# Kernel optimization log

Hardware: AMD Instinct MI355X
Metric: run time of the kernel (lower is better)

The kernel has to match this reference:

```python
import jax, jax.numpy as jnp
import numpy as np
from jax import lax


def setup_inputs() -> dict:
    key = jax.random.key(0)
    ks = jax.random.split(key, 5)
    D, S, T, B, H = 2, 48, 48, 32, 256
    std = 1.0 / np.sqrt(H)
    return {
        "src_input_seq": jax.random.normal(ks[0], (S, B, H), jnp.float32),
        "trg_input_seq": jax.random.normal(ks[1], (T, B, H), jnp.float32),
        "W": jax.random.uniform(ks[2], (D, H, H), jnp.float32, -std, std),
        "U": jax.random.uniform(ks[3], (D, 2 * H, H), jnp.float32, -std, std),
        "b": jax.random.uniform(ks[4], (D, 1, H), jnp.float32, -std, std),
    }


def _grid_layer(x, y, Wd, Ud, bd):
    # x, y: [S, T, B, H] per-cell inputs for this depth
    S, T, B, H = x.shape
    Ux, Uy = Ud[:H], Ud[H:]  # state = concat([state_x, state_y]) @ U

    def row_step(prev_row_hx, row_inputs):
        # prev_row_hx: [T, B, H] = h_x of row i-1 (state_x); zeros for i == 0
        x_row, y_row = row_inputs  # [T, B, H]

        def cell_step(left_hx, inp):
            # left_hx: [B, H] = h_x of cell (i, j-1) (state_y); zeros for j == 0
            up_hx, x_t, y_t = inp
            temp = up_hx @ Ux + left_hx @ Uy + bd  # [B, H]
            h_x = jnp.tanh(x_t @ Wd + temp)
            h_y = jnp.tanh(y_t @ Wd + temp)
            return h_x, (h_x, h_y)

        _, (hx_row, hy_row) = lax.scan(
            cell_step, jnp.zeros((B, H), x.dtype), (prev_row_hx, x_row, y_row)
        )
        return hx_row, (hx_row, hy_row)

    _, (HX, HY) = lax.scan(row_step, jnp.zeros((T, B, H), x.dtype), (x, y))
    return jnp.stack([HX, HY], axis=2)  # [S, T, 2, B, H]


def reference(src_input_seq, trg_input_seq, W, U, b):
    S, B, H = src_input_seq.shape
    T = trg_input_seq.shape[0]
    depth = W.shape[0]
    # depth-0 inputs: x_t = src[i] (same for all j), y_t = trg[j] (same for all i)
    xs = jnp.broadcast_to(src_input_seq[:, None], (S, T, B, H))
    ys = jnp.broadcast_to(trg_input_seq[None, :], (S, T, B, H))
    outs = []
    for d in range(depth):
        Hd = _grid_layer(xs, ys, W[d], U[d], b[d])  # [S, T, 2, B, H]
        outs.append(Hd)
        xs, ys = Hd[:, :, 0], Hd[:, :, 1]
    return jnp.stack(outs, axis=0)  # [depth, S, T, 2, B, H]
```

## Files before the change

### kernel.cpp

```cpp
#include <hip/hip_runtime.h>
#include <hip/hip_bf16.h>


typedef short short8 __attribute__((ext_vector_type(8)));
typedef float f32x4 __attribute__((ext_vector_type(4)));

static constexpr size_t UF_OFF    = 0;
static constexpr size_t WF_OFF    = 512u * 1024;
static constexpr size_t SRCW_OFF  = 768u * 1024;
static constexpr size_t TRGW_OFF  = SRCW_OFF + 48u * 32 * 256 * 4;
static constexpr size_t FLAG0_OFF = TRGW_OFF + 48u * 32 * 256 * 4;
static constexpr size_t FLAG1_OFF = FLAG0_OFF + 48u * 48 * 4;

#define MFMA16(a, b, c) __builtin_amdgcn_mfma_f32_16x16x32_bf16(a, b, c, 0, 0, 0)

__device__ __forceinline__ short f2bf(float f) {
  __hip_bfloat16 h = __float2bfloat16(f);
  return __builtin_bit_cast(short, h);
}

__device__ __forceinline__ size_t plane_off(int d, int s, int t, int c) {
  return (size_t)(((d * 48 + s) * 48 + t) * 2 + c) * 8192u;
}

__device__ __forceinline__ void wait_ge(int* p, int v) {
  while (__hip_atomic_load(p, __ATOMIC_RELAXED, __HIP_MEMORY_SCOPE_AGENT) < v)
    __builtin_amdgcn_s_sleep(1);
  asm volatile("" ::: "memory");
}

__device__ __forceinline__ void st_llc(float* p, float v) {
  __hip_atomic_store(p, v, __ATOMIC_RELAXED, __HIP_MEMORY_SCOPE_AGENT);
}

__device__ __forceinline__ float fast_tanh(float x) {
  float e = exp2f(x * 2.88539008f);
  return 1.f - __fdividef(2.f, e + 1.f);
}

__global__ void preswizzle(const float* __restrict__ U,
                           const float* __restrict__ W,
                           char* __restrict__ ws) {
  int gid = blockIdx.x * 256 + threadIdx.x;
  if (gid < 32768) {
    int r = gid >> 11;
    int d = r >> 3, nh = (r >> 2) & 1, w = r & 3;
    int c = gid & 2047;
    int f = c >> 6, lane = c & 63;
    int nt = f >> 4, ks = f & 15;
    int kbase = ks * 32 + (lane >> 4) * 8;
    int n = nh * 128 + w * 32 + nt * 16 + (lane & 15);
    const float* sp = U + (size_t)d * 512 * 256 + n;
    short8 v;
#pragma unroll
    for (int j = 0; j < 8; ++j) v[j] = f2bf(sp[(size_t)(kbase + j) * 256]);
    *(short8*)(ws + UF_OFF + (size_t)gid * 16) = v;
  } else {
    int idx = gid - 32768;
    int r = idx >> 10;
    int d = r >> 3, nh = (r >> 2) & 1, w = r & 3;
    int c = idx & 1023;
    int f = c >> 6, lane = c & 63;
    int nt = f >> 3, ks = f & 7;
    int kbase = ks * 32 + (lane >> 4) * 8;
    int n = nh * 128 + w * 32 + nt * 16 + (lane & 15);
    const float* sp = W + (size_t)d * 256 * 256 + n;
    short8 v;
#pragma unroll
    for (int j = 0; j < 8; ++j) v[j] = f2bf(sp[(size_t)(kbase + j) * 256]);
    *(short8*)(ws + WF_OFF + (size_t)idx * 16) = v;
  }
}

__global__ __launch_bounds__(256, 1) void precompute_xw(
    const float* __restrict__ src, const float* __restrict__ trg,
    const float* __restrict__ bvec, char* __restrict__ ws) {
  __shared__ __align__(16) char lds[32 * 528];
  const int bid = blockIdx.x;
  const int i = bid >> 1, nh = bid & 1;
  const int tid = threadIdx.x;
  const int w = tid >> 6, lane = tid & 63;
  const int alane = lane & 15, q = lane >> 4;

  short8 bw[2][8];
  {
    const char* wb = ws + WF_OFF + (size_t)(nh * 4 + w) * 16384u + (size_t)lane * 16;
#pragma unroll
    for (int nt = 0; nt < 2; ++nt)
#pragma unroll
      for (int ks = 0; ks < 8; ++ks)
        bw[nt][ks] = *(const short8*)(wb + (nt * 8 + ks) * 1024);
  }

  const float* plane = (i < 48) ? src + (size_t)i * 8192 : trg + (size_t)(i - 48) * 8192;
#pragma unroll
  for (int it = 0; it < 4; ++it) {
    int gid = it * 256 + tid;
    int row = gid >> 5, c = gid & 31;
    const float* p = plane + row * 256 + c * 8;
    short8 v;
#pragma unroll
    for (int j = 0; j < 8; ++j) v[j] = f2bf(p[j]);
    *(short8*)(lds + row * 528 + c * 16) = v;
  }
  __syncthreads();

  const f32x4 zf = {0.f, 0.f, 0.f, 0.f};
  f32x4 acc[2][2];
  acc[0][0] = zf; acc[0][1] = zf; acc[1][0] = zf; acc[1][1] = zf;
  const char* ar0 = lds + alane * 528 + q * 16;
  const char* ar1 = lds + (alane + 16) * 528 + q * 16;
#pragma unroll
  for (int ks = 0; ks < 8; ++ks) {
    short8 a0 = *(const short8*)(ar0 + ks * 64);
    short8 a1 = *(const short8*)(ar1 + ks * 64);
#pragma unroll
    for (int nt = 0; nt < 2; ++nt) {
      acc[0][nt] = MFMA16(a0, bw[nt][ks], acc[0][nt]);
      acc[1][nt] = MFMA16(a1, bw[nt][ks], acc[1][nt]);
    }
  }

  const int n0 = nh * 128 + w * 32 + alane;
  float bs[2] = {bvec[n0], bvec[n0 + 16]};
  float* dst = (float*)(ws + (i < 48 ? SRCW_OFF : TRGW_OFF)) +
               (size_t)(i < 48 ? i : i - 48) * 8192;
#pragma unroll
  for (int mt = 0; mt < 2; ++mt)
#pragma unroll
    for (int nt = 0; nt < 2; ++nt)
#pragma unroll
      for (int rr = 0; rr < 4; ++rr) {
        int row = mt * 16 + q * 4 + rr;
        dst[row * 256 + n0 + nt * 16] = acc[mt][nt][rr] + bs[nt];
      }
}

__global__ __launch_bounds__(256, 1) void grid_main(
    float* __restrict__ out, const float* __restrict__ bvec,
    char* __restrict__ ws) {
  __shared__ __align__(16) char lds[32 * 1040];
  const int bid = blockIdx.x;
  const int d = bid / 96;
  const int r = bid % 96;
  const int t = r >> 1, nh = r & 1;
  const int tid = threadIdx.x;
  const int w = tid >> 6, lane = tid & 63;
  const int alane = lane & 15, q = lane >> 4;

  int* flag0 = (int*)(ws + FLAG0_OFF);
  int* flag1 = (int*)(ws + FLAG1_OFF);
  const float* SRCW = (const float*)(ws + SRCW_OFF);
  const float* TRGW = (const float*)(ws + TRGW_OFF);

  short8 bu[2][16];
  {
    const char* ub = ws + UF_OFF + (size_t)((d * 2 + nh) * 4 + w) * 32768u + (size_t)lane * 16;
#pragma unroll
    for (int nt = 0; nt < 2; ++nt)
#pragma unroll
      for (int ks = 0; ks < 16; ++ks)
        bu[nt][ks] = *(const short8*)(ub + (nt * 16 + ks) * 1024);
  }
  short8 bw[2][8];
  float bs1[2] = {0.f, 0.f};
  if (d == 1) {
    const char* wb = ws + WF_OFF + (size_t)((2 + nh) * 4 + w) * 16384u + (size_t)lane * 16;
#pragma unroll
    for (int nt = 0; nt < 2; ++nt)
#pragma unroll
      for (int ks = 0; ks < 8; ++ks)
        bw[nt][ks] = *(const short8*)(wb + (nt * 8 + ks) * 1024);
    int bn = nh * 128 + w * 32 + alane;
    bs1[0] = bvec[256 + bn];
    bs1[1] = bvec[256 + bn + 16];
  }

  const char* ar0 = lds + alane * 1040 + q * 16;
  const char* ar1 = lds + (alane + 16) * 1040 + q * 16;
  const int n0 = nh * 128 + w * 32 + alane;
  const f32x4 zf = {0.f, 0.f, 0.f, 0.f};

  for (int s = 0; s < 48; ++s) {
    f32x4 acc[2][2];
    acc[0][0] = zf; acc[0][1] = zf; acc[1][0] = zf; acc[1][1] = zf;

    if (d == 0) {
      float pfx[16], pfy[16];
      {
        const float* sxp = SRCW + (size_t)s * 8192;
        const float* syp = TRGW + (size_t)t * 8192;
#pragma unroll
        for (int mt = 0; mt < 2; ++mt)
#pragma unroll
          for (int nt = 0; nt < 2; ++nt)
#pragma unroll
            for (int rr = 0; rr < 4; ++rr) {
              int row = mt * 16 + q * 4 + rr;
              int n = n0 + nt * 16;
              pfx[(mt * 2 + nt) * 4 + rr] = sxp[row * 256 + n];
              pfy[(mt * 2 + nt) * 4 + rr] = syp[row * 256 + n];
            }
      }
      if (s > 0) wait_ge(&flag0[(s - 1) * 48 + t], 2);
      if (t > 0) wait_ge(&flag0[s * 48 + (t - 1)], 2);
      {
        const float* pu = (s > 0) ? out + plane_off(0, s - 1, t, 0) : nullptr;
        const float* pl = (t > 0) ? out + plane_off(0, s, t - 1, 0) : nullptr;
#pragma unroll
        for (int it = 0; it < 8; ++it) {
          int gid = it * 256 + tid;
          int p = gid >> 10, row = (gid >> 5) & 31, c = gid & 31;
          const float* pp = p ? pl : pu;
          short8 v = {0, 0, 0, 0, 0, 0, 0, 0};
          if (pp) {
#pragma unroll
            for (int j = 0; j < 8; ++j) v[j] = f2bf(pp[row * 256 + c * 8 + j]);
          }
          *(short8*)(lds + row * 1040 + (p * 32 + c) * 16) = v;
        }
      }
      __syncthreads();
#pragma unroll
      for (int ks = 0; ks < 16; ++ks) {
        short8 a0 = *(const short8*)(ar0 + ks * 64);
        short8 a1 = *(const short8*)(ar1 + ks * 64);
#pragma unroll
        for (int nt = 0; nt < 2; ++nt) {
          acc[0][nt] = MFMA16(a0, bu[nt][ks], acc[0][nt]);
          acc[1][nt] = MFMA16(a1, bu[nt][ks], acc[1][nt]);
        }
      }
      float* hxp = out + plane_off(0, s, t, 0);
      float* hyp = out + plane_off(0, s, t, 1);
#pragma unroll
      for (int mt = 0; mt < 2; ++mt)
#pragma unroll
        for (int nt = 0; nt < 2; ++nt)
#pragma unroll
          for (int rr = 0; rr < 4; ++rr) {
            int row = mt * 16 + q * 4 + rr;
            int n = n0 + nt * 16;
            int i = (mt * 2 + nt) * 4 + rr;
            float tv = acc[mt][nt][rr];
            st_llc(&hxp[row * 256 + n], fast_tanh(pfx[i] + tv));
            st_llc(&hyp[row * 256 + n], fast_tanh(pfy[i] + tv));
          }
    } else {
      wait_ge(&flag0[s * 48 + t], 2);
      {
        const float* px = out + plane_off(0, s, t, 0);
        const float* py = out + plane_off(0, s, t, 1);
#pragma unroll
        for (int it = 0; it < 8; ++it) {
          int gid = it * 256 + tid;
          int p = gid >> 10, row = (gid >> 5) & 31, c = gid & 31;
          const float* pp = p ? py : px;
          short8 v;
#pragma unroll
          for (int j = 0; j < 8; ++j) v[j] = f2bf(pp[row * 256 + c * 8 + j]);
          *(short8*)(lds + row * 1040 + (p * 32 + c) * 16) = v;
        }
      }
      __syncthreads();
      f32x4 accx[2][2], accy[2][2];
      accx[0][0] = zf; accx[0][1] = zf; accx[1][0] = zf; accx[1][1] = zf;
      accy[0][0] = zf; accy[0][1] = zf; accy[1][0] = zf; accy[1][1] = zf;
#pragma unroll
      for (int ks = 0; ks < 8; ++ks) {
        short8 ax0 = *(const short8*)(ar0 + ks * 64);
        short8 ax1 = *(const short8*)(ar1 + ks * 64);
        short8 ay0 = *(const short8*)(ar0 + 512 + ks * 64);
        short8 ay1 = *(const short8*)(ar1 + 512 + ks * 64);
#pragma unroll
        for (int nt = 0; nt < 2; ++nt) {
          accx[0][nt] = MFMA16(ax0, bw[nt][ks], accx[0][nt]);
          accx[1][nt] = MFMA16(ax1, bw[nt][ks], accx[1][nt]);
          accy[0][nt] = MFMA16(ay0, bw[nt][ks], accy[0][nt]);
          accy[1][nt] = MFMA16(ay1, bw[nt][ks], accy[1][nt]);
        }
      }
      __syncthreads();
      if (s > 0) wait_ge(&flag1[(s - 1) * 48 + t], 2);
      if (t > 0) wait_ge(&flag1[s * 48 + (t - 1)], 2);
      {
        const float* pu = (s > 0) ? out + plane_off(1, s - 1, t, 0) : nullptr;
        const float* pl = (t > 0) ? out + plane_off(1, s, t - 1, 0) : nullptr;
#pragma unroll
        for (int it = 0; it < 8; ++it) {
          int gid = it * 256 + tid;
          int p = gid >> 10, row = (gid >> 5) & 31, c = gid & 31;
          const float* pp = p ? pl : pu;
          short8 v = {0, 0, 0, 0, 0, 0, 0, 0};
          if (pp) {
#pragma unroll
            for (int j = 0; j < 8; ++j) v[j] = f2bf(pp[row * 256 + c * 8 + j]);
          }
          *(short8*)(lds + row * 1040 + (p * 32 + c) * 16) = v;
        }
      }
      __syncthreads();
#pragma unroll
      for (int ks = 0; ks < 16; ++ks) {
        short8 a0 = *(const short8*)(ar0 + ks * 64);
        short8 a1 = *(const short8*)(ar1 + ks * 64);
#pragma unroll
        for (int nt = 0; nt < 2; ++nt) {
          acc[0][nt] = MFMA16(a0, bu[nt][ks], acc[0][nt]);
          acc[1][nt] = MFMA16(a1, bu[nt][ks], acc[1][nt]);
        }
      }
      float* hxp = out + plane_off(1, s, t, 0);
      float* hyp = out + plane_off(1, s, t, 1);
#pragma unroll
      for (int mt = 0; mt < 2; ++mt)
#pragma unroll
        for (int nt = 0; nt < 2; ++nt)
#pragma unroll
          for (int rr = 0; rr < 4; ++rr) {
            int row = mt * 16 + q * 4 + rr;
            int n = n0 + nt * 16;
            float tv = acc[mt][nt][rr];
            st_llc(&hxp[row * 256 + n], fast_tanh(accx[mt][nt][rr] + tv + bs1[nt]));
            hyp[row * 256 + n] = fast_tanh(accy[mt][nt][rr] + tv + bs1[nt]);
          }
    }
    asm volatile("s_waitcnt vmcnt(0)" ::: "memory");
    __syncthreads();
    if (tid == 0) {
      int* fp = (d == 0) ? &flag0[s * 48 + t] : &flag1[s * 48 + t];
      __hip_atomic_fetch_add(fp, 1, __ATOMIC_RELAXED, __HIP_MEMORY_SCOPE_AGENT);
    }
  }
}

extern "C" void kernel_launch(void* const* d_in, const int* in_sizes, int n_in,
                              void* d_out, int out_size, void* d_ws, size_t ws_size,
                              hipStream_t stream) {
  const float* src = (const float*)d_in[0];
  const float* trg = (const float*)d_in[1];
  const float* W   = (const float*)d_in[2];
  const float* U   = (const float*)d_in[3];
  const float* bv  = (const float*)d_in[4];
  float* out = (float*)d_out;
  char* ws = (char*)d_ws;

  hipMemsetAsync(ws + FLAG0_OFF, 0, 2u * 48 * 48 * 4, stream);
  preswizzle<<<192, 256, 0, stream>>>(U, W, ws);
  precompute_xw<<<192, 256, 0, stream>>>(src, trg, bv, ws);
  grid_main<<<192, 256, 0, stream>>>(out, bv, ws);
}
```

Measured before the change: 964.5 us.

## Merge column halves into one block and keep the up-state in LDS

Each block now owns a whole t-column (both N halves, 512 threads) instead of half of one. The block keeps its own previous-row h_x in LDS as bf16, so only the left neighbour has to be fetched from global memory after a flag wait. Flags are padded to separate cache lines and counted per wave (8 arrivals). Depth-1 W fragments are read from global inside the loop rather than held in registers. This shortens the cross-block dependency chain and halves the global traffic per cell. The cost is fewer blocks (96) and heavier per-block work, including duplicated MFMAs for the x and y accumulators at depth 0.

```diff
diff --git a/kernel.cpp b/kernel.cpp
--- a/kernel.cpp
+++ b/kernel.cpp
@@ -10,7 +10,8 @@
 static constexpr size_t SRCW_OFF  = 768u * 1024;
 static constexpr size_t TRGW_OFF  = SRCW_OFF + 48u * 32 * 256 * 4;
 static constexpr size_t FLAG0_OFF = TRGW_OFF + 48u * 32 * 256 * 4;
-static constexpr size_t FLAG1_OFF = FLAG0_OFF + 48u * 48 * 4;
+static constexpr size_t FLAG1_OFF = FLAG0_OFF + 48u * 48 * 128;
+static constexpr int    FSTRIDE   = 32;
 
 #define MFMA16(a, b, c) __builtin_amdgcn_mfma_f32_16x16x32_bf16(a, b, c, 0, 0, 0)
 
@@ -136,60 +137,127 @@
       }
 }
 
-__global__ __launch_bounds__(256, 1) void grid_main(
+__global__ __launch_bounds__(512, 2) void grid_main(
     float* __restrict__ out, const float* __restrict__ bvec,
     char* __restrict__ ws) {
-  __shared__ __align__(16) char lds[32 * 1040];
+  __shared__ __align__(16) char lds[3 * 32 * 528];
+  char* const buf0 = lds;
+  char* const buf1 = lds + 32 * 528;
+  char* const buf2 = lds + 2 * 32 * 528;
+
   const int bid = blockIdx.x;
-  const int d = bid / 96;
-  const int r = bid % 96;
-  const int t = r >> 1, nh = r & 1;
+  const int d = bid / 48;
+  const int t = bid % 48;
   const int tid = threadIdx.x;
-  const int w = tid >> 6, lane = tid & 63;
+  const int wv = tid >> 6;
+  const int nh = wv >> 2, w = wv & 3;
+  const int lane = tid & 63;
   const int alane = lane & 15, q = lane >> 4;
+  const int n0 = nh * 128 + w * 32 + alane;
 
   int* flag0 = (int*)(ws + FLAG0_OFF);
   int* flag1 = (int*)(ws + FLAG1_OFF);
   const float* SRCW = (const float*)(ws + SRCW_OFF);
   const float* TRGW = (const float*)(ws + TRGW_OFF);
 
+  for (int i = tid; i < 32 * 528 / 4; i += 512) ((int*)buf0)[i] = 0;
+
   short8 bu[2][16];
   {
-    const char* ub = ws + UF_OFF + (size_t)((d * 2 + nh) * 4 + w) * 32768u + (size_t)lane * 16;
+    const char* ub = ws + UF_OFF + (size_t)((d * 2 + nh) * 4 + w) * 32768u +
+                     (size_t)lane * 16;
 #pragma unroll
     for (int nt = 0; nt < 2; ++nt)
 #pragma unroll
       for (int ks = 0; ks < 16; ++ks)
         bu[nt][ks] = *(const short8*)(ub + (nt * 16 + ks) * 1024);
   }
-  short8 bw[2][8];
-  float bs1[2] = {0.f, 0.f};
-  if (d == 1) {
-    const char* wb = ws + WF_OFF + (size_t)((2 + nh) * 4 + w) * 16384u + (size_t)lane * 16;
-#pragma unroll
-    for (int nt = 0; nt < 2; ++nt)
-#pragma unroll
-      for (int ks = 0; ks < 8; ++ks)
-        bw[nt][ks] = *(const short8*)(wb + (nt * 8 + ks) * 1024);
-    int bn = nh * 128 + w * 32 + alane;
-    bs1[0] = bvec[256 + bn];
-    bs1[1] = bvec[256 + bn + 16];
-  }
-
-  const char* ar0 = lds + alane * 1040 + q * 16;
-  const char* ar1 = lds + (alane + 16) * 1040 + q * 16;
-  const int n0 = nh * 128 + w * 32 + alane;
-  const f32x4 zf = {0.f, 0.f, 0.f, 0.f};
-
-  for (int s = 0; s < 48; ++s) {
-    f32x4 acc[2][2];
-    acc[0][0] = zf; acc[0][1] = zf; acc[1][0] = zf; acc[1][1] = zf;
-
-    if (d == 0) {
-      float pfx[16], pfy[16];
+
+  const char* up0 = buf0 + alane * 528 + q * 16;
+  const char* up1 = buf0 + (alane + 16) * 528 + q * 16;
+  const char* l0  = buf1 + alane * 528 + q * 16;
+  const char* l1  = buf1 + (alane + 16) * 528 + q * 16;
+  const char* y0  = buf2 + alane * 528 + q * 16;
+  const char* y1  = buf2 + (alane + 16) * 528 + q * 16;
+
+  __syncthreads();
+
+  if (d == 0) {
+    float pfy[16];
+    {
+      const float* syp = TRGW + (size_t)t * 8192;
+#pragma unroll
+      for (int mt = 0; mt < 2; ++mt)
+#pragma unroll
+        for (int nt = 0; nt < 2; ++nt)
+#pragma unroll
+          for (int rr = 0; rr < 4; ++rr) {
+            int row = mt * 16 + q * 4 + rr;
+            pfy[(mt * 2 + nt) * 4 + rr] = syp[row * 256 + n0 + nt * 16];
+          }
+    }
+    for (int s = 0; s < 48; ++s) {
+      f32x4 accx[2][2], accy[2][2];
       {
         const float* sxp = SRCW + (size_t)s * 8192;
-        const float* syp = TRGW + (size_t)t * 8192;
+#pragma unroll
+        for (int mt = 0; mt < 2; ++mt)
+#pragma unroll
+          for (int nt = 0; nt < 2; ++nt)
+#pragma unroll
+            for (int rr = 0; rr < 4; ++rr) {
+              int row = mt * 16 + q * 4 + rr;
+              accx[mt][nt][rr] = sxp[row * 256 + n0 + nt * 16];
+              accy[mt][nt][rr] = pfy[(mt * 2 + nt) * 4 + rr];
+            }
+      }
+      if (t > 0) {
+        wait_ge(&flag0[(s * 48 + (t - 1)) * FSTRIDE], 8);
+        const float* pl = out + plane_off(0, s, t - 1, 0);
+#pragma unroll
+        for (int it = 0; it < 2; ++it) {
+          int gid = it * 512 + tid;
+          int row = gid >> 5, c = gid & 31;
+          const float* p = pl + row * 256 + c * 8;
+          short8 v;
+#pragma unroll
+          for (int j = 0; j < 8; ++j) v[j] = f2bf(p[j]);
+          *(short8*)(buf1 + row * 528 + c * 16) = v;
+        }
+      }
+      __syncthreads();
+#pragma unroll
+      for (int ks = 0; ks < 8; ++ks) {
+        short8 a0 = *(const short8*)(up0 + ks * 64);
+        short8 a1 = *(const short8*)(up1 + ks * 64);
+        accx[0][0] = MFMA16(a0, bu[0][ks], accx[0][0]);
+        accx[0][1] = MFMA16(a0, bu[1][ks], accx[0][1]);
+        accx[1][0] = MFMA16(a1, bu[0][ks], accx[1][0]);
+        accx[1][1] = MFMA16(a1, bu[1][ks], accx[1][1]);
+        accy[0][0] = MFMA16(a0, bu[0][ks], accy[0][0]);
+        accy[0][1] = MFMA16(a0, bu[1][ks], accy[0][1]);
+        accy[1][0] = MFMA16(a1, bu[0][ks], accy[1][0]);
+        accy[1][1] = MFMA16(a1, bu[1][ks], accy[1][1]);
+      }
+      if (t > 0) {
+#pragma unroll
+        for (int ks = 0; ks < 8; ++ks) {
+          short8 a0 = *(const short8*)(l0 + ks * 64);
+          short8 a1 = *(const short8*)(l1 + ks * 64);
+          accx[0][0] = MFMA16(a0, bu[0][8 + ks], accx[0][0]);
+          accx[0][1] = MFMA16(a0, bu[1][8 + ks], accx[0][1]);
+          accx[1][0] = MFMA16(a1, bu[0][8 + ks], accx[1][0]);
+          accx[1][1] = MFMA16(a1, bu[1][8 + ks], accx[1][1]);
+          accy[0][0] = MFMA16(a0, bu[0][8 + ks], accy[0][0]);
+          accy[0][1] = MFMA16(a0, bu[1][8 + ks], accy[0][1]);
+          accy[1][0] = MFMA16(a1, bu[0][8 + ks], accy[1][0]);
+          accy[1][1] = MFMA16(a1, bu[1][8 + ks], accy[1][1]);
+        }
+      }
+      float hx[16];
+      {
+        float* hxp = out + plane_off(0, s, t, 0);
+        float* hyp = out + plane_off(0, s, t, 1);
 #pragma unroll
         for (int mt = 0; mt < 2; ++mt)
 #pragma unroll
@@ -198,41 +266,18 @@
             for (int rr = 0; rr < 4; ++rr) {
               int row = mt * 16 + q * 4 + rr;
               int n = n0 + nt * 16;
-              pfx[(mt * 2 + nt) * 4 + rr] = sxp[row * 256 + n];
-              pfy[(mt * 2 + nt) * 4 + rr] = syp[row * 256 + n];
+              float xv = fast_tanh(accx[mt][nt][rr]);
+              float yv = fast_tanh(accy[mt][nt][rr]);
+              hx[(mt * 2 + nt) * 4 + rr] = xv;
+              st_llc(&hxp[row * 256 + n], xv);
+              st_llc(&hyp[row * 256 + n], yv);
             }
       }
-      if (s > 0) wait_ge(&flag0[(s - 1) * 48 + t], 2);
-      if (t > 0) wait_ge(&flag0[s * 48 + (t - 1)], 2);
-      {
-        const float* pu = (s > 0) ? out + plane_off(0, s - 1, t, 0) : nullptr;
-        const float* pl = (t > 0) ? out + plane_off(0, s, t - 1, 0) : nullptr;
-#pragma unroll
-        for (int it = 0; it < 8; ++it) {
-          int gid = it * 256 + tid;
-          int p = gid >> 10, row = (gid >> 5) & 31, c = gid & 31;
-          const float* pp = p ? pl : pu;
-          short8 v = {0, 0, 0, 0, 0, 0, 0, 0};
-          if (pp) {
-#pragma unroll
-            for (int j = 0; j < 8; ++j) v[j] = f2bf(pp[row * 256 + c * 8 + j]);
-          }
-          *(short8*)(lds + row * 1040 + (p * 32 + c) * 16) = v;
-        }
-      }
-      __syncthreads();
-#pragma unroll
-      for (int ks = 0; ks < 16; ++ks) {
-        short8 a0 = *(const short8*)(ar0 + ks * 64);
-        short8 a1 = *(const short8*)(ar1 + ks * 64);
-#pragma unroll
-        for (int nt = 0; nt < 2; ++nt) {
-          acc[0][nt] = MFMA16(a0, bu[nt][ks], acc[0][nt]);
-          acc[1][nt] = MFMA16(a1, bu[nt][ks], acc[1][nt]);
-        }
-      }
-      float* hxp = out + plane_off(0, s, t, 0);
-      float* hyp = out + plane_off(0, s, t, 1);
+      asm volatile("s_waitcnt vmcnt(0)" ::: "memory");
+      if (lane == 0)
+        __hip_atomic_fetch_add(&flag0[(s * 48 + t) * FSTRIDE], 1,
+                               __ATOMIC_RELAXED, __HIP_MEMORY_SCOPE_AGENT);
+      __syncthreads();
 #pragma unroll
       for (int mt = 0; mt < 2; ++mt)
 #pragma unroll
@@ -240,78 +285,120 @@
 #pragma unroll
           for (int rr = 0; rr < 4; ++rr) {
             int row = mt * 16 + q * 4 + rr;
-            int n = n0 + nt * 16;
-            int i = (mt * 2 + nt) * 4 + rr;
-            float tv = acc[mt][nt][rr];
-            st_llc(&hxp[row * 256 + n], fast_tanh(pfx[i] + tv));
-            st_llc(&hyp[row * 256 + n], fast_tanh(pfy[i] + tv));
+            *(short*)(buf0 + row * 528 + (n0 + nt * 16) * 2) =
+                f2bf(hx[(mt * 2 + nt) * 4 + rr]);
           }
-    } else {
-      wait_ge(&flag0[s * 48 + t], 2);
+      __syncthreads();
+    }
+  } else {
+    const char* wb = ws + WF_OFF + (size_t)((2 + nh) * 4 + w) * 16384u +
+                     (size_t)lane * 16;
+    const float bsa = bvec[256 + n0], bsb = bvec[256 + n0 + 16];
+    const f32x4 bA = {bsa, bsa, bsa, bsa};
+    const f32x4 bB = {bsb, bsb, bsb, bsb};
+    const f32x4 zf = {0.f, 0.f, 0.f, 0.f};
+    for (int s = 0; s < 48; ++s) {
+      f32x4 accx[2][2], accy[2][2], acc[2][2];
+      accx[0][0] = bA; accx[0][1] = bB; accx[1][0] = bA; accx[1][1] = bB;
+      accy[0][0] = bA; accy[0][1] = bB; accy[1][0] = bA; accy[1][1] = bB;
+      acc[0][0] = zf; acc[0][1] = zf; acc[1][0] = zf; acc[1][1] = zf;
+
+      wait_ge(&flag0[(s * 48 + t) * FSTRIDE], 8);
       {
         const float* px = out + plane_off(0, s, t, 0);
         const float* py = out + plane_off(0, s, t, 1);
 #pragma unroll
-        for (int it = 0; it < 8; ++it) {
-          int gid = it * 256 + tid;
-          int p = gid >> 10, row = (gid >> 5) & 31, c = gid & 31;
-          const float* pp = p ? py : px;
+        for (int it = 0; it < 4; ++it) {
+          int gid = it * 512 + tid;
+          int pidx = gid >> 10, row = (gid >> 5) & 31, c = gid & 31;
+          const float* pp = pidx ? py : px;
+          char* db = pidx ? buf2 : buf1;
+          const float* p = pp + row * 256 + c * 8;
           short8 v;
 #pragma unroll
-          for (int j = 0; j < 8; ++j) v[j] = f2bf(pp[row * 256 + c * 8 + j]);
-          *(short8*)(lds + row * 1040 + (p * 32 + c) * 16) = v;
+          for (int j = 0; j < 8; ++j) v[j] = f2bf(p[j]);
+          *(short8*)(db + row * 528 + c * 16) = v;
         }
       }
       __syncthreads();
-      f32x4 accx[2][2], accy[2][2];
-      accx[0][0] = zf; accx[0][1] = zf; accx[1][0] = zf; accx[1][1] = zf;
-      accy[0][0] = zf; accy[0][1] = zf; accy[1][0] = zf; accy[1][1] = zf;
 #pragma unroll
       for (int ks = 0; ks < 8; ++ks) {
-        short8 ax0 = *(const short8*)(ar0 + ks * 64);
-        short8 ax1 = *(const short8*)(ar1 + ks * 64);
-        short8 ay0 = *(const short8*)(ar0 + 512 + ks * 64);
-        short8 ay1 = *(const short8*)(ar1 + 512 + ks * 64);
-#pragma unroll
-        for (int nt = 0; nt < 2; ++nt) {
-          accx[0][nt] = MFMA16(ax0, bw[nt][ks], accx[0][nt]);
-          accx[1][nt] = MFMA16(ax1, bw[nt][ks], accx[1][nt]);
-          accy[0][nt] = MFMA16(ay0, bw[nt][ks], accy[0][nt]);
-          accy[1][nt] = MFMA16(ay1, bw[nt][ks], accy[1][nt]);
+        short8 b0 = *(const short8*)(wb + ks * 1024);
+        short8 b1 = *(const short8*)(wb + (8 + ks) * 1024);
+        short8 ax0 = *(const short8*)(l0 + ks * 64);
+        short8 ax1 = *(const short8*)(l1 + ks * 64);
+        short8 ay0 = *(const short8*)(y0 + ks * 64);
+        short8 ay1 = *(const short8*)(y1 + ks * 64);
+        accx[0][0] = MFMA16(ax0, b0, accx[0][0]);
+        accx[0][1] = MFMA16(ax0, b1, accx[0][1]);
+        accx[1][0] = MFMA16(ax1, b0, accx[1][0]);
+        accx[1][1] = MFMA16(ax1, b1, accx[1][1]);
+        accy[0][0] = MFMA16(ay0, b0, accy[0][0]);
+        accy[0][1] = MFMA16(ay0, b1, accy[0][1]);
+        accy[1][0] = MFMA16(ay1, b0, accy[1][0]);
+        accy[1][1] = MFMA16(ay1, b1, accy[1][1]);
+      }
+      if (t > 0) wait_ge(&flag1[(s * 48 + (t - 1)) * FSTRIDE], 8);
+      __syncthreads();
+      if (t > 0) {
+        const float* pl = out + plane_off(1, s, t - 1, 0);
+#pragma unroll
+        for (int it = 0; it < 2; ++it) {
+          int gid = it * 512 + tid;
+          int row = gid >> 5, c = gid & 31;
+          const float* p = pl + row * 256 + c * 8;
+          short8 v;
+#pragma unroll
+          for (int j = 0; j < 8; ++j) v[j] = f2bf(p[j]);
+          *(short8*)(buf1 + row * 528 + c * 16) = v;
         }
       }
       __syncthreads();
-      if (s > 0) wait_ge(&flag1[(s - 1) * 48 + t], 2);
-      if (t > 0) wait_ge(&flag1[s * 48 + (t - 1)], 2);
+#pragma unroll
+      for (int ks = 0; ks < 8; ++ks) {
+        short8 a0 = *(const short8*)(up0 + ks * 64);
+        short8 a1 = *(const short8*)(up1 + ks * 64);
+        acc[0][0] = MFMA16(a0, bu[0][ks], acc[0][0]);
+        acc[0][1] = MFMA16(a0, bu[1][ks], acc[0][1]);
+        acc[1][0] = MFMA16(a1, bu[0][ks], acc[1][0]);
+        acc[1][1] = MFMA16(a1, bu[1][ks], acc[1][1]);
+      }
+      if (t > 0) {
+#pragma unroll
+        for (int ks = 0; ks < 8; ++ks) {
+          short8 a0 = *(const short8*)(l0 + ks * 64);
+          short8 a1 = *(const short8*)(l1 + ks * 64);
+          acc[0][0] = MFMA16(a0, bu[0][8 + ks], acc[0][0]);
+          acc[0][1] = MFMA16(a0, bu[1][8 + ks], acc[0][1]);
+          acc[1][0] = MFMA16(a1, bu[0][8 + ks], acc[1][0]);
+          acc[1][1] = MFMA16(a1, bu[1][8 + ks], acc[1][1]);
+        }
+      }
+      float hx[16];
       {
-        const float* pu = (s > 0) ? out + plane_off(1, s - 1, t, 0) : nullptr;
-        const float* pl = (t > 0) ? out + plane_off(1, s, t - 1, 0) : nullptr;
-#pragma unroll
-        for (int it = 0; it < 8; ++it) {
-          int gid = it * 256 + tid;
-          int p = gid >> 10, row = (gid >> 5) & 31, c = gid & 31;
-          const float* pp = p ? pl : pu;
-          short8 v = {0, 0, 0, 0, 0, 0, 0, 0};
-          if (pp) {
-#pragma unroll
-            for (int j = 0; j < 8; ++j) v[j] = f2bf(pp[row * 256 + c * 8 + j]);
-          }
-          *(short8*)(lds + row * 1040 + (p * 32 + c) * 16) = v;
-        }
-      }
-      __syncthreads();
-#pragma unroll
-      for (int ks = 0; ks < 16; ++ks) {
-        short8 a0 = *(const short8*)(ar0 + ks * 64);
-        short8 a1 = *(const short8*)(ar1 + ks * 64);
-#pragma unroll
-        for (int nt = 0; nt < 2; ++nt) {
-          acc[0][nt] = MFMA16(a0, bu[nt][ks], acc[0][nt]);
-          acc[1][nt] = MFMA16(a1, bu[nt][ks], acc[1][nt]);
-        }
-      }
-      float* hxp = out + plane_off(1, s, t, 0);
-      float* hyp = out + plane_off(1, s, t, 1);
+        float* hxp = out + plane_off(1, s, t, 0);
+        float* hyp = out + plane_off(1, s, t, 1);
+#pragma unroll
+        for (int mt = 0; mt < 2; ++mt)
+#pragma unroll
+          for (int nt = 0; nt < 2; ++nt)
+#pragma unroll
+            for (int rr = 0; rr < 4; ++rr) {
+              int row = mt * 16 + q * 4 + rr;
+              int n = n0 + nt * 16;
+              float tv = acc[mt][nt][rr];
+              float xv = fast_tanh(accx[mt][nt][rr] + tv);
+              float yv = fast_tanh(accy[mt][nt][rr] + tv);
+              hx[(mt * 2 + nt) * 4 + rr] = xv;
+              st_llc(&hxp[row * 256 + n], xv);
+              hyp[row * 256 + n] = yv;
+            }
+      }
+      asm volatile("s_waitcnt vmcnt(0)" ::: "memory");
+      if (lane == 0)
+        __hip_atomic_fetch_add(&flag1[(s * 48 + t) * FSTRIDE], 1,
+                               __ATOMIC_RELAXED, __HIP_MEMORY_SCOPE_AGENT);
+      __syncthreads();
 #pragma unroll
       for (int mt = 0; mt < 2; ++mt)
 #pragma unroll
@@ -319,17 +406,10 @@
 #pragma unroll
           for (int rr = 0; rr < 4; ++rr) {
             int row = mt * 16 + q * 4 + rr;
-            int n = n0 + nt * 16;
-            float tv = acc[mt][nt][rr];
-            st_llc(&hxp[row * 256 + n], fast_tanh(accx[mt][nt][rr] + tv + bs1[nt]));
-            hyp[row * 256 + n] = fast_tanh(accy[mt][nt][rr] + tv + bs1[nt]);
+            *(short*)(buf0 + row * 528 + (n0 + nt * 16) * 2) =
+                f2bf(hx[(mt * 2 + nt) * 4 + rr]);
           }
-    }
-    asm volatile("s_waitcnt vmcnt(0)" ::: "memory");
-    __syncthreads();
-    if (tid == 0) {
-      int* fp = (d == 0) ? &flag0[s * 48 + t] : &flag1[s * 48 + t];
-      __hip_atomic_fetch_add(fp, 1, __ATOMIC_RELAXED, __HIP_MEMORY_SCOPE_AGENT);
+      __syncthreads();
     }
   }
 }
@@ -345,8 +425,8 @@
   float* out = (float*)d_out;
   char* ws = (char*)d_ws;
 
-  hipMemsetAsync(ws + FLAG0_OFF, 0, 2u * 48 * 48 * 4, stream);
+  hipMemsetAsync(ws + FLAG0_OFF, 0, 2u * 48 * 48 * 128, stream);
   preswizzle<<<192, 256, 0, stream>>>(U, W, ws);
   precompute_xw<<<192, 256, 0, stream>>>(src, trg, bv, ws);
-  grid_main<<<192, 256, 0, stream>>>(out, bv, ws);
-}
+  grid_main<<<96, 512, 0, stream>>>(out, bv, ws);
+}
```

Result: faster. 901.8 us (-6.5%).
